# Kernel tuning notes

Hardware: AMD Instinct MI355X
Metric: run time of the kernel (lower is better)

## Reference

```python
import jax, jax.numpy as jnp
import numpy as np

B, L, T = 16, 256, 256
ENC, DEC, MEL, SPK = 256, 1024, 80, 256
ATT, FILT, K = 128, 32, 31


def setup_inputs() -> dict:
    key = jax.random.key(0)
    ks = jax.random.split(key, 32)
    s = 0.05
    r = lambda k, shape: jax.random.normal(k, shape, dtype=jnp.float32) * s
    return {
        'encoder_outputs': jax.random.normal(ks[0], (B, L, ENC), dtype=jnp.float32),
        'speaker_embed': jax.random.normal(ks[1], (B, SPK), dtype=jnp.float32),
        'mels': jax.random.normal(ks[2], (B, T, MEL), dtype=jnp.float32),
        # prenet
        'W_pre1': r(ks[3], (DEC, MEL)), 'b_pre1': jnp.zeros((DEC,), jnp.float32),
        'W_pre2': r(ks[4], (DEC, DEC)), 'b_pre2': jnp.zeros((DEC,), jnp.float32),
        # speaker projection
        'W_sp': r(ks[5], (DEC, SPK)), 'b_sp': jnp.zeros((DEC,), jnp.float32),
        # location-sensitive attention (Tacotron-2 style)
        'W_q': r(ks[6], (ATT, DEC)),
        'W_m': r(ks[7], (ATT, ENC)),
        'W_loc_conv': r(ks[8], (FILT, 2, K)),
        'W_loc': r(ks[9], (ATT, FILT)),
        'v_att': r(ks[10], (ATT,)),
        # LSTM cells
        'W_ih1': r(ks[11], (4 * DEC, DEC + ENC)), 'W_hh1': r(ks[12], (4 * DEC, DEC)),
        'b_ih1': jnp.zeros((4 * DEC,), jnp.float32), 'b_hh1': jnp.zeros((4 * DEC,), jnp.float32),
        'W_ih2': r(ks[13], (4 * DEC, DEC)), 'W_hh2': r(ks[14], (4 * DEC, DEC)),
        'b_ih2': jnp.zeros((4 * DEC,), jnp.float32), 'b_hh2': jnp.zeros((4 * DEC,), jnp.float32),
        # output projections
        'W_mel': r(ks[15], (MEL, DEC)), 'b_mel': jnp.zeros((MEL,), jnp.float32),
        'W_stop': r(ks[16], (1, DEC)), 'b_stop': jnp.zeros((1,), jnp.float32),
    }


def _lstm_cell(x, h, c, W_ih, W_hh, b_ih, b_hh):
    g = x @ W_ih.T + h @ W_hh.T + b_ih + b_hh
    i, f, gg, o = jnp.split(g, 4, axis=-1)
    c2 = jax.nn.sigmoid(f) * c + jax.nn.sigmoid(i) * jnp.tanh(gg)
    h2 = jax.nn.sigmoid(o) * jnp.tanh(c2)
    return h2, c2


def reference(encoder_outputs, speaker_embed, mels,
              W_pre1, b_pre1, W_pre2, b_pre2, W_sp, b_sp,
              W_q, W_m, W_loc_conv, W_loc, v_att,
              W_ih1, W_hh1, b_ih1, b_hh1, W_ih2, W_hh2, b_ih2, b_hh2,
              W_mel, b_mel, W_stop, b_stop):
    b = encoder_outputs.shape[0]
    proc_mem = jnp.einsum('bld,ad->bla', encoder_outputs, W_m)  # [B,L,ATT]
    spk = speaker_embed @ W_sp.T + b_sp                          # [B,DEC]
    # teacher forcing: step 0 uses zeros, step i>0 uses mels[:, i] (matches torch loop)
    prev_mel_seq = jnp.concatenate([jnp.zeros_like(mels[:, :1]), mels[:, 1:]], axis=1)
    prev_mel_seq = prev_mel_seq.transpose(1, 0, 2)               # [T,B,MEL]

    def step(carry, prev_mel):
        h1, c1, h2, c2, prev_w, cum_w = carry
        # prenet (dropout = identity in eval)
        p = jax.nn.relu(prev_mel @ W_pre1.T + b_pre1)
        p = jax.nn.relu(p @ W_pre2.T + b_pre2)
        q = p + spk
        # location features over [prev, cumulative] attention weights
        loc = jnp.stack([prev_w, cum_w], axis=1)                 # [B,2,L]
        f = jax.lax.conv_general_dilated(loc, W_loc_conv, (1,), [(K // 2, K // 2)],
                                         dimension_numbers=('NCH', 'OIH', 'NCH'))  # [B,FILT,L]
        e = jnp.einsum('bla,a->bl', jnp.tanh((q @ W_q.T)[:, None, :]
                                             + jnp.einsum('bcl,ac->bla', f, W_loc)
                                             + proc_mem), v_att)  # [B,L]
        w = jax.nn.softmax(e, axis=1)
        ctx = jnp.einsum('bl,bld->bd', w, encoder_outputs)        # [B,ENC]
        h1n, c1n = _lstm_cell(jnp.concatenate([p, ctx], axis=1), h1, c1, W_ih1, W_hh1, b_ih1, b_hh1)
        h2n, c2n = _lstm_cell(h1n, h2, c2, W_ih2, W_hh2, b_ih2, b_hh2)
        mel = h2n @ W_mel.T + b_mel
        stop = jax.nn.sigmoid(h2n @ W_stop.T + b_stop)
        return (h1n, c1n, h2n, c2n, w, cum_w + w), (mel, stop)

    z = lambda d: jnp.zeros((b, d), jnp.float32)
    carry0 = (z(DEC), z(DEC), z(DEC), z(DEC), z(L), z(L))
    _, (mel_seq, stop_seq) = jax.lax.scan(step, carry0, prev_mel_seq)
    return mel_seq.transpose(1, 0, 2), stop_seq.transpose(1, 0, 2)
```

## Files before the change

kernel.cpp:

```cpp
#include <hip/hip_runtime.h>


namespace {

constexpr int TT = 256, BB = 16, LL = 256, MELD = 80, FILTD = 32, KC = 31;
constexpr int P1 = 2304;
constexpr int P2 = 2048;
constexpr int REDOFF = 32768;

typedef float f32x4 __attribute__((ext_vector_type(4)));

struct Args {
  const float *enc, *spe, *mels;
  const float *Wpre1, *bpre1, *Wpre2, *bpre2, *Wsp, *bsp;
  const float *Wq, *Wm, *Wconv, *Wloc, *vatt;
  const float *Wih1, *Whh1, *bih1, *bhh1;
  const float *Wih2, *Whh2, *bih2, *bhh2;
  const float *Wmel, *bmel, *Wstop, *bstop;
  float *p, *X, *qp2, *pm2, *prevmel;
  float *h1a, *h1b, *c1, *h2a, *h2b, *c2;
  float *cum, *wexp, *uctx, *pctx, *psum, *spkvec, *spkq;
  float *W81, *b81, *tmp;
  int *slots, *epoch, *pslots, *pepoch;
  float *out;
};

__device__ __forceinline__ float fast_tanh(float x) {
  float ax = fabsf(x);
  float e = __expf(-2.f * ax);
  float t = (1.f - e) / (1.f + e);
  return copysignf(t, x);
}
__device__ __forceinline__ float fast_sig(float x) { return 1.f / (1.f + __expf(-x)); }

__device__ __forceinline__ int cldi(const int* p) {
  int v;
  asm volatile("global_load_dword %0, %1, off sc0 sc1\n\ts_waitcnt vmcnt(0)"
               : "=v"(v) : "v"(p) : "memory");
  return v;
}
__device__ __forceinline__ void cst1(float* p, float v) {
  asm volatile("global_store_dword %0, %1, off sc0 sc1" :: "v"(p), "v"(v) : "memory");
}
__device__ __forceinline__ void csti(int* p, int v) {
  asm volatile("global_store_dword %0, %1, off sc0 sc1" :: "v"(p), "v"(v) : "memory");
}

__device__ __forceinline__ void bar_lgkm() {
  asm volatile("s_waitcnt lgkmcnt(0)" ::: "memory");
  __builtin_amdgcn_s_barrier();
  __builtin_amdgcn_sched_barrier(0);
}

__device__ __forceinline__ void glls(const float* g, float* l) {
  __builtin_amdgcn_global_load_lds((const __attribute__((address_space(1))) void*)g,
                                   (__attribute__((address_space(3))) void*)l, 16, 0, 0);
}

__device__ __forceinline__ void gridbar(int* slots, int* epoch, int target) {
  __syncthreads();
  if (blockIdx.x == 0) {
    if (threadIdx.x == 0) csti(&slots[0], target);
    while (cldi(&slots[threadIdx.x * 32]) < target) __builtin_amdgcn_s_sleep(1);
    __syncthreads();
    if (threadIdx.x == 0) csti(epoch, target);
  } else {
    if (threadIdx.x == 0) {
      csti(&slots[blockIdx.x * 32], target);
      while (cldi(epoch) < target) __builtin_amdgcn_s_sleep(8);
    }
  }
  __builtin_amdgcn_fence(__ATOMIC_ACQUIRE, "agent");
  __syncthreads();
}

__global__ void k_init(float* base, int n) {
  int i = blockIdx.x * blockDim.x + threadIdx.x;
  if (i < n) base[i] = 0.f;
}

__global__ void k_setpsum(float* psum) {
  if (threadIdx.x < 16) psum[256 + threadIdx.x * 16] = 1.f;
}

__global__ void k_prevmel(Args a) {
  int i = blockIdx.x * blockDim.x + threadIdx.x;
  if (i >= TT * BB * MELD) return;
  int m = i % MELD;
  int tb = i / MELD;
  int b = tb & 15, t = tb >> 4;
  a.prevmel[i] = (t == 0) ? 0.f : a.mels[(b * TT + t) * MELD + m];
}

__global__ void k_spkvec(Args a) {
  int i = blockIdx.x * blockDim.x + threadIdx.x;
  if (i >= BB * 1024) return;
  int b = i >> 10, j = i & 1023;
  const float* x = a.spe + b * 256;
  const float* w = a.Wsp + j * 256;
  float s = a.bsp[j];
  for (int k = 0; k < 256; ++k) s += x[k] * w[k];
  a.spkvec[i] = s;
}

__global__ void k_spkq(Args a) {
  int i = blockIdx.x * blockDim.x + threadIdx.x;
  if (i >= BB * 128) return;
  int b = i >> 7, q = i & 127;
  const float* x = a.spkvec + b * 1024;
  const float* w = a.Wq + q * 1024;
  float s = 0.f;
  for (int k = 0; k < 1024; ++k) s += x[k] * w[k];
  a.spkq[i] = s;
}

__global__ void k_prep81(Args a) {
  int i = blockIdx.x * blockDim.x + threadIdx.x;
  if (i < 81 * 1024) {
    int r = i >> 10, k = i & 1023;
    a.W81[i] = (r < 80) ? a.Wmel[r * 1024 + k] : a.Wstop[k];
  }
  if (i < 81) a.b81[i] = (i < 80) ? a.bmel[i] : a.bstop[0];
}

__global__ __launch_bounds__(256) void k_gemm(const float* __restrict__ A,
                                              const float* __restrict__ Bm,
                                              const float* __restrict__ bias,
                                              float* __restrict__ C,
                                              int M, int N, int K, int act) {
  __shared__ __align__(16) float As[16][132];
  __shared__ __align__(16) float Bs[16][68];
  const int bm = blockIdx.y * 128, bn = blockIdx.x * 64;
  const int tid = threadIdx.x;
  const int tm = (tid >> 4) * 8, tn = (tid & 15) * 4;
  float acc[8][4] = {};
  for (int k0 = 0; k0 < K; k0 += 16) {
    for (int i = tid; i < 512; i += 256) {
      int m = i >> 2, kq = i & 3;
      float4 v = *(const float4*)(A + (size_t)(bm + m) * K + k0 + kq * 4);
      As[kq * 4 + 0][m] = v.x; As[kq * 4 + 1][m] = v.y;
      As[kq * 4 + 2][m] = v.z; As[kq * 4 + 3][m] = v.w;
    }
    {
      int m = tid >> 2, kq = tid & 3;
      float4 v = *(const float4*)(Bm + (size_t)(bn + m) * K + k0 + kq * 4);
      Bs[kq * 4 + 0][m] = v.x; Bs[kq * 4 + 1][m] = v.y;
      Bs[kq * 4 + 2][m] = v.z; Bs[kq * 4 + 3][m] = v.w;
    }
    __syncthreads();
#pragma unroll
    for (int kk = 0; kk < 16; ++kk) {
      float4 a0 = *(const float4*)&As[kk][tm];
      float4 a1 = *(const float4*)&As[kk][tm + 4];
      float4 b0 = *(const float4*)&Bs[kk][tn];
      float av[8] = {a0.x, a0.y, a0.z, a0.w, a1.x, a1.y, a1.z, a1.w};
      float bv[4] = {b0.x, b0.y, b0.z, b0.w};
#pragma unroll
      for (int i = 0; i < 8; ++i)
#pragma unroll
        for (int j = 0; j < 4; ++j) acc[i][j] += av[i] * bv[j];
    }
    __syncthreads();
  }
#pragma unroll
  for (int i = 0; i < 8; ++i)
#pragma unroll
    for (int j = 0; j < 4; ++j) {
      float v = acc[i][j];
      if (bias) v += bias[bn + tn + j];
      if (act == 1) v = fmaxf(v, 0.f);
      C[(size_t)(bm + tm + i) * N + bn + tn + j] = v;
    }
}

__global__ void k_pm_transpose(Args a) {
  int i = blockIdx.x * blockDim.x + threadIdx.x;
  if (i >= BB * 128 * LL) return;
  int l = i & 255;
  int rest = i >> 8;
  int q = rest & 127, b = rest >> 7;
  a.pm2[i] = a.X[(size_t)((b << 8) + l) * 128 + q];
}

__global__ void k_addspkq(Args a) {
  int i = blockIdx.x * blockDim.x + threadIdx.x;
  if (i >= TT * BB * 128) return;
  int q = i & 127, b = (i >> 7) & 15;
  a.qp2[i] += a.spkq[b * 128 + q];
}

__global__ __launch_bounds__(256, 1) void k_persist(Args a) {
  __shared__ __align__(16) float xs[16 * P1];
  __shared__ __align__(16) float asc[720];
  __shared__ __align__(16) float gbuf2[280];
  const int wg = blockIdx.x, tid = threadIdx.x;
  const int wv = tid >> 6, lane = tid & 63;
  const int d0 = wg * 4, kl = lane * 4;
  const int ag = tid & 15, ll = tid >> 4;

  float* loc0 = asc;
  float* loc1 = asc + 64;
  float* aF   = asc + 128;
  float* expv = asc + 704;

  float4 wL1[9][4];
  float4 wL2[8][4];
#pragma unroll
  for (int q = 0; q < 4; ++q) {
    const int row = wv * 1024 + d0 + q;
    const float* rih1 = a.Wih1 + (size_t)row * 1280;
    const float* rhh1 = a.Whh1 + (size_t)row * 1024;
    const float* rih2 = a.Wih2 + (size_t)row * 1024;
    const float* rhh2 = a.Whh2 + (size_t)row * 1024;
#pragma unroll
    for (int kb = 0; kb < 9; ++kb)
      wL1[kb][q] = (kb < 5) ? *(const float4*)(rih1 + kb * 256 + kl)
                            : *(const float4*)(rhh1 + kb * 256 + kl - 1280);
#pragma unroll
    for (int kb = 0; kb < 8; ++kb)
      wL2[kb][q] = (kb < 4) ? *(const float4*)(rih2 + kb * 256 + kl)
                            : *(const float4*)(rhh2 + kb * 256 + kl - 1024);
  }
  const int row_r = wv * 1024 + d0 + (lane >> 4);
  const float bsum1 = a.bih1[row_r] + a.bhh1[row_r];
  const float bsum2 = a.bih2[row_r] + a.bhh2[row_r];

  const int bH = wg >> 4, cH = wg & 15, l0H = cH << 4, lH = l0H + ll;
  float pmv[8], va[8];
  {
    const float* pmb = a.pm2 + (size_t)bH * 32768;
#pragma unroll
    for (int j = 0; j < 8; ++j) {
      pmv[j] = pmb[(size_t)(ag * 8 + j) * 256 + lH];
      va[j] = a.vatt[ag * 8 + j];
    }
  }
  float ev[16];
  {
    const float* eb = a.enc + (size_t)((bH << 8) + l0H) * 256 + tid;
#pragma unroll
    for (int l2 = 0; l2 < 16; ++l2) ev[l2] = eb[l2 * 256];
  }

  float c1v = 0.f, c2v = 0.f;
  __syncthreads();

  for (int t = 0; t < 259; ++t) {
    const int cur = t & 1, prv = cur ^ 1;

    if (wg < 16 && t >= 1 && t <= 256) {
      const int par = (t - 1) & 1, b = wg;
      float sm;
      {
        const f32x4* ps4 = (const f32x4*)(a.psum + par * 256 + b * 16);
        f32x4 p0 = ps4[0], p1 = ps4[1], p2 = ps4[2], p3 = ps4[3];
        sm = (p0[0] + p0[1] + p0[2] + p0[3]) + (p1[0] + p1[1] + p1[2] + p1[3]) +
             (p2[0] + p2[1] + p2[2] + p2[3]) + (p3[0] + p3[1] + p3[2] + p3[3]);
      }
      const float inv = 1.f / sm;
      const float* pc = a.pctx + par * 65536 + b * 4096 + tid;
      float acc = 0.f;
#pragma unroll
      for (int i = 0; i < 16; ++i) acc += pc[i * 256];
      cst1(a.uctx + par * 4096 + b * 256 + tid, acc * inv);
    }

    float qpm[8], wf[8];
    if (t < 256) {
      float sm;
      {
        const f32x4* ps4 = (const f32x4*)(a.psum + prv * 256 + bH * 16);
        f32x4 p0 = ps4[0], p1 = ps4[1], p2 = ps4[2], p3 = ps4[3];
        sm = (p0[0] + p0[1] + p0[2] + p0[3]) + (p1[0] + p1[1] + p1[2] + p1[3]) +
             (p2[0] + p2[1] + p2[2] + p2[3]) + (p3[0] + p3[1] + p3[2] + p3[3]);
      }
      const float inv_ps = 1.f / sm;
      {
        const float* qpb = a.qp2 + ((size_t)(t << 4) + bH) * 128 + ag * 8;
        float4 q0 = *(const float4*)qpb;
        float4 q1 = *(const float4*)(qpb + 4);
        qpm[0] = q0.x + pmv[0]; qpm[1] = q0.y + pmv[1];
        qpm[2] = q0.z + pmv[2]; qpm[3] = q0.w + pmv[3];
        qpm[4] = q1.x + pmv[4]; qpm[5] = q1.y + pmv[5];
        qpm[6] = q1.z + pmv[6]; qpm[7] = q1.w + pmv[7];
      }
      if (tid < 64) {
        int lp = l0H - 16 + tid;
        bool ok = (lp >= 0 && lp < LL);
        float we = 0.f, cm = 0.f;
        if (ok) {
          we = a.wexp[prv * 4096 + bH * 256 + lp];
          cm = a.cum[prv * 4096 + bH * 256 + lp];
        }
        float wn = we * inv_ps;
        loc0[tid] = wn;
        loc1[tid] = ok ? (cm + wn) : 0.f;
      }
      bar_lgkm();
      if (tid < 16) cst1(a.cum + cur * 4096 + bH * 256 + l0H + tid, loc1[16 + tid]);
      for (int idx = tid; idx < FILTD * 16; idx += 256) {
        int fc = idx >> 4, ll2 = idx & 15;
        const float* w = a.Wconv + fc * 62;
        float s = 0.f;
#pragma unroll
        for (int k = 0; k < KC; ++k) {
          s += w[k] * loc0[ll2 + k + 1];
          s += w[31 + k] * loc1[ll2 + k + 1];
        }
        aF[ll2 * 36 + fc] = s;
      }
      bar_lgkm();
      {
        const float* ftr = aF + ll * 36;
        f32x4 f[8];
#pragma unroll
        for (int c4 = 0; c4 < 8; ++c4) f[c4] = *(const f32x4*)(ftr + c4 * 4);
#pragma unroll
        for (int j = 0; j < 8; ++j) {
          const float* wl = a.Wloc + (ag * 8 + j) * 32;
          float x = 0.f;
#pragma unroll
          for (int c4 = 0; c4 < 8; ++c4) {
            float4 w4 = *(const float4*)(wl + c4 * 4);
            x += w4.x * f[c4][0] + w4.y * f[c4][1] + w4.z * f[c4][2] + w4.w * f[c4][3];
          }
          wf[j] = x;
        }
      }
    }

    if (t >= 2 && t <= 257) {
      const int s1 = t - 2;
      const float* pt = a.p + (size_t)s1 * 16384;
      const float* h1r = (s1 & 1) ? a.h1a : a.h1b;
      const float* uc = a.uctx + (size_t)(s1 & 1) * 4096;
#pragma unroll
      for (int k = 0; k < 16; ++k)
        glls(pt + (size_t)(tid + k * 256) * 4, xs + k * P1 + wv * 256);
#pragma unroll
      for (int k = 0; k < 4; ++k)
        glls(uc + (size_t)(tid + k * 256) * 4, xs + (k * 4 + wv) * P1 + 1024);
#pragma unroll
      for (int k = 0; k < 16; ++k)
        glls(h1r + (size_t)(tid + k * 256) * 4, xs + k * P1 + 1280 + wv * 256);
    }

    if (t < 256) {
      {
        float s = 0.f;
#pragma unroll
        for (int j = 0; j < 8; ++j) s += va[j] * fast_tanh(qpm[j] + wf[j]);
        s += __shfl_down(s, 8, 16);
        s += __shfl_down(s, 4, 16);
        s += __shfl_down(s, 2, 16);
        s += __shfl_down(s, 1, 16);
        if (ag == 0) {
          float ex = __expf(s);
          expv[ll] = ex;
          cst1(a.wexp + cur * 4096 + bH * 256 + lH, ex);
        }
      }
      bar_lgkm();
      if (tid == 0) {
        float s = 0.f;
#pragma unroll
        for (int i = 0; i < 16; ++i) s += expv[i];
        cst1(a.psum + cur * 256 + bH * 16 + cH, s);
      }
      {
        float sctx = 0.f;
#pragma unroll
        for (int l2 = 0; l2 < 16; ++l2) sctx += expv[l2] * ev[l2];
        cst1(a.pctx + cur * 65536 + (bH * 16 + cH) * 256 + tid, sctx);
      }
    }

    if (t >= 2 && t <= 257) {
      __syncthreads();
      float acc[4][16];
#pragma unroll
      for (int q = 0; q < 4; ++q)
#pragma unroll
        for (int b = 0; b < 16; ++b) acc[q][b] = 0.f;
#pragma unroll
      for (int kb = 0; kb < 9; ++kb) {
        const float* xb = xs + kb * 256 + kl;
#pragma unroll
        for (int b = 0; b < 16; ++b) {
          float4 x4 = *(const float4*)(xb + b * P1);
#pragma unroll
          for (int q = 0; q < 4; ++q) {
            acc[q][b] += wL1[kb][q].x * x4.x;
            acc[q][b] += wL1[kb][q].y * x4.y;
            acc[q][b] += wL1[kb][q].z * x4.z;
            acc[q][b] += wL1[kb][q].w * x4.w;
          }
        }
      }
#pragma unroll
      for (int q = 0; q < 4; ++q)
#pragma unroll
        for (int b = 0; b < 16; ++b) {
          float v = acc[q][b];
          v += __shfl_xor(v, 32);
          v += __shfl_xor(v, 16);
          acc[q][b] = v;
        }
      bar_lgkm();
      if (lane < 16) {
        float* rb = xs + REDOFF + wv * 1024 + lane * 64;
        const int sx = lane << 2;
#pragma unroll
        for (int q = 0; q < 4; ++q)
#pragma unroll
          for (int bg = 0; bg < 4; ++bg) {
            f32x4 v = {acc[q][bg * 4 + 0], acc[q][bg * 4 + 1],
                       acc[q][bg * 4 + 2], acc[q][bg * 4 + 3]};
            *(f32x4*)(rb + ((q * 16 + bg * 4) ^ sx)) = v;
          }
      }
    }

    if (t >= 3) {
      const int s2 = t - 3;
      const float* h1s = (s2 & 1) ? a.h1b : a.h1a;
      const float* h2r = (s2 & 1) ? a.h2a : a.h2b;
#pragma unroll
      for (int k = 0; k < 16; ++k)
        glls(h1s + (size_t)(tid + k * 256) * 4, xs + k * P2 + wv * 256);
#pragma unroll
      for (int k = 0; k < 16; ++k)
        glls(h2r + (size_t)(tid + k * 256) * 4, xs + k * P2 + 1024 + wv * 256);
    }

    if (t >= 2 && t <= 257) {
      float* h1w = ((t - 2) & 1) ? a.h1b : a.h1a;
      {
        const int lo = lane & ~3, li = lane & 3;
        const float* rbase = xs + REDOFF + wv * 1024;
        float g = bsum1;
#pragma unroll
        for (int k = 0; k < 16; ++k) g += rbase[k * 64 + (lo ^ (k << 2)) + li];
        gbuf2[wv * 68 + lane] = g;
      }
      bar_lgkm();
      if (tid < 64) {
        int dd = tid >> 4, b = tid & 15, d = d0 + dd;
        float gi = gbuf2[0 * 68 + tid], gf = gbuf2[1 * 68 + tid];
        float gg = gbuf2[2 * 68 + tid], go = gbuf2[3 * 68 + tid];
        float cn = fast_sig(gf) * c1v + fast_sig(gi) * fast_tanh(gg);
        float hn = fast_sig(go) * fast_tanh(cn);
        c1v = cn;
        cst1(h1w + b * 1024 + d, hn);
      }
    }

    if (t >= 3) {
      const int s2 = t - 3;
      float* h2w = (s2 & 1) ? a.h2b : a.h2a;
      __syncthreads();
      float acc[4][16];
#pragma unroll
      for (int q = 0; q < 4; ++q)
#pragma unroll
        for (int b = 0; b < 16; ++b) acc[q][b] = 0.f;
#pragma unroll
      for (int kb = 0; kb < 8; ++kb) {
        const float* xb = xs + kb * 256 + kl;
#pragma unroll
        for (int b = 0; b < 16; ++b) {
          float4 x4 = *(const float4*)(xb + b * P2);
#pragma unroll
          for (int q = 0; q < 4; ++q) {
            acc[q][b] += wL2[kb][q].x * x4.x;
            acc[q][b] += wL2[kb][q].y * x4.y;
            acc[q][b] += wL2[kb][q].z * x4.z;
            acc[q][b] += wL2[kb][q].w * x4.w;
          }
        }
      }
#pragma unroll
      for (int q = 0; q < 4; ++q)
#pragma unroll
        for (int b = 0; b < 16; ++b) {
          float v = acc[q][b];
          v += __shfl_xor(v, 32);
          v += __shfl_xor(v, 16);
          acc[q][b] = v;
        }
      if (lane < 16) {
        float* rb = xs + REDOFF + wv * 1024 + lane * 64;
        const int sx = lane << 2;
#pragma unroll
        for (int q = 0; q < 4; ++q)
#pragma unroll
          for (int bg = 0; bg < 4; ++bg) {
            f32x4 v = {acc[q][bg * 4 + 0], acc[q][bg * 4 + 1],
                       acc[q][bg * 4 + 2], acc[q][bg * 4 + 3]};
            *(f32x4*)(rb + ((q * 16 + bg * 4) ^ sx)) = v;
          }
      }
      {
        const int lo = lane & ~3, li = lane & 3;
        const float* rbase = xs + REDOFF + wv * 1024;
        float g = bsum2;
#pragma unroll
        for (int k = 0; k < 16; ++k) g += rbase[k * 64 + (lo ^ (k << 2)) + li];
        gbuf2[wv * 68 + lane] = g;
      }
      bar_lgkm();
      if (tid < 64) {
        int dd = tid >> 4, b = tid & 15, d = d0 + dd;
        float gi = gbuf2[0 * 68 + tid], gf = gbuf2[1 * 68 + tid];
        float gg = gbuf2[2 * 68 + tid], go = gbuf2[3 * 68 + tid];
        float cn = fast_sig(gf) * c2v + fast_sig(gi) * fast_tanh(gg);
        float hn = fast_sig(go) * fast_tanh(cn);
        c2v = cn;
        cst1(h2w + b * 1024 + d, hn);
        a.X[(size_t)(s2 * 16 + b) * 1024 + d] = hn;
      }
    }

    if (t < 258) gridbar(a.slots, a.epoch, t + 1);
  }
}

__global__ void k_finish(Args a) {
  int i = blockIdx.x * blockDim.x + threadIdx.x;
  if (i >= 4096 * 128) return;
  int col = i & 127, tb = i >> 7;
  int t = tb >> 4, b = tb & 15;
  float v = a.tmp[i];
  if (col < 80) a.out[(size_t)(b * 256 + t) * 80 + col] = v;
  else if (col == 80) a.out[327680 + b * 256 + t] = fast_sig(v);
}

}

extern "C" void kernel_launch(void* const* d_in, const int* in_sizes, int n_in,
                              void* d_out, int out_size, void* d_ws, size_t ws_size,
                              hipStream_t stream) {
  float* ws = (float*)d_ws;
  Args a;
  a.enc = (const float*)d_in[0];
  a.spe = (const float*)d_in[1];
  a.mels = (const float*)d_in[2];
  a.Wpre1 = (const float*)d_in[3];  a.bpre1 = (const float*)d_in[4];
  a.Wpre2 = (const float*)d_in[5];  a.bpre2 = (const float*)d_in[6];
  a.Wsp = (const float*)d_in[7];    a.bsp = (const float*)d_in[8];
  a.Wq = (const float*)d_in[9];     a.Wm = (const float*)d_in[10];
  a.Wconv = (const float*)d_in[11]; a.Wloc = (const float*)d_in[12];
  a.vatt = (const float*)d_in[13];
  a.Wih1 = (const float*)d_in[14];  a.Whh1 = (const float*)d_in[15];
  a.bih1 = (const float*)d_in[16];  a.bhh1 = (const float*)d_in[17];
  a.Wih2 = (const float*)d_in[18];  a.Whh2 = (const float*)d_in[19];
  a.bih2 = (const float*)d_in[20];  a.bhh2 = (const float*)d_in[21];
  a.Wmel = (const float*)d_in[22];  a.bmel = (const float*)d_in[23];
  a.Wstop = (const float*)d_in[24]; a.bstop = (const float*)d_in[25];

  a.p    = ws + 0;
  a.X    = ws + 4194304;
  a.qp2  = ws + 8388608;
  a.pm2  = ws + 8912896;
  float* st = ws + 9437184;
  a.h1a = st + 0;      a.h1b = st + 16384;
  a.c1  = st + 32768;
  a.h2a = st + 49152;  a.h2b = st + 65536;
  a.c2  = st + 81920;
  a.cum  = st + 98304;
  a.wexp = st + 106496;
  a.uctx = st + 114688;
  a.pctx = st + 122880;
  a.psum = st + 253952;
  a.slots  = (int*)(st + 254464);
  a.epoch  = (int*)(st + 262656);
  a.pslots = (int*)(st + 262688);
  a.pepoch = (int*)(st + 270880);
  a.spkvec = ws + 9708096;
  a.spkq   = ws + 9724480;
  a.W81    = ws + 9726528;
  a.b81    = ws + 9857600;
  a.tmp    = ws + 9857728;
  a.prevmel = a.tmp;
  a.out = (float*)d_out;

  k_init<<<(270912 + 255) / 256, 256, 0, stream>>>(st, 270912);
  k_setpsum<<<1, 64, 0, stream>>>(a.psum);
  k_prevmel<<<(TT * BB * MELD + 255) / 256, 256, 0, stream>>>(a);
  k_spkvec<<<(BB * 1024 + 255) / 256, 256, 0, stream>>>(a);
  k_spkq<<<(BB * 128 + 255) / 256, 256, 0, stream>>>(a);
  k_prep81<<<(81 * 1024 + 255) / 256, 256, 0, stream>>>(a);

  k_gemm<<<dim3(16, 32), 256, 0, stream>>>(a.prevmel, a.Wpre1, a.bpre1, a.X, 4096, 1024, 80, 1);
  k_gemm<<<dim3(16, 32), 256, 0, stream>>>(a.X, a.Wpre2, a.bpre2, a.p, 4096, 1024, 1024, 1);
  k_gemm<<<dim3(2, 32), 256, 0, stream>>>(a.p, a.Wq, nullptr, a.qp2, 4096, 128, 1024, 0);
  k_addspkq<<<(TT * BB * 128 + 255) / 256, 256, 0, stream>>>(a);
  k_gemm<<<dim3(2, 32), 256, 0, stream>>>(a.enc, a.Wm, nullptr, a.X, 4096, 128, 256, 0);
  k_pm_transpose<<<(BB * 128 * LL + 255) / 256, 256, 0, stream>>>(a);

  {
    void* kargs[] = {(void*)&a};
    hipError_t e = hipLaunchCooperativeKernel(reinterpret_cast<const void*>(&k_persist),
                                              dim3(256), dim3(256), kargs, 0, stream);
    if (e != hipSuccess) k_persist<<<256, 256, 0, stream>>>(a);
  }

  k_gemm<<<dim3(2, 32), 256, 0, stream>>>(a.X, a.W81, a.b81, a.tmp, 4096, 128, 1024, 0);
  k_finish<<<(4096 * 128 + 255) / 256, 256, 0, stream>>>(a);
}
```

Before: 15.37 ms.

## Use 32-deep ring buffers for recurrent state to skip most grid-barrier acquire fences

Replaces the double-buffered h1/h2/uctx/psum state with 32-slot ring buffers indexed by timestep. The per-step agent-scope acquire fence (cache invalidate) in the grid barrier now runs only every 16 steps. Cross-block reads of pctx, wexp and cum switch to coherent sc0/sc1 loads so they stay fresh without the fence. The aim is to cut cache-invalidation cost on every step of the persistent kernel. The risk is correctness: any remaining cached (non-coherent) read of data written by another block, such as the plain psum loads, could return stale values between fences.

```diff
diff --git a/kernel.cpp b/kernel.cpp
--- a/kernel.cpp
+++ b/kernel.cpp
@@ -18,10 +18,10 @@
   const float *Wih2, *Whh2, *bih2, *bhh2;
   const float *Wmel, *bmel, *Wstop, *bstop;
   float *p, *X, *qp2, *pm2, *prevmel;
-  float *h1a, *h1b, *c1, *h2a, *h2b, *c2;
-  float *cum, *wexp, *uctx, *pctx, *psum, *spkvec, *spkq;
+  float *cum, *wexp, *pctx, *spkvec, *spkq;
+  float *h1d, *h2d, *uctxd, *psumd;
   float *W81, *b81, *tmp;
-  int *slots, *epoch, *pslots, *pepoch;
+  int *slots, *epoch;
   float *out;
 };
 
@@ -45,6 +45,34 @@
 __device__ __forceinline__ void csti(int* p, int v) {
   asm volatile("global_store_dword %0, %1, off sc0 sc1" :: "v"(p), "v"(v) : "memory");
 }
+__device__ __forceinline__ void cld2(float* d0, float* d1, const float* q0,
+                                     const float* q1) {
+  float x, y;
+  asm volatile(
+      "global_load_dword %0, %2, off sc0 sc1\n\t"
+      "global_load_dword %1, %3, off sc0 sc1\n\t"
+      "s_waitcnt vmcnt(0)"
+      : "=&v"(x), "=&v"(y) : "v"(q0), "v"(q1) : "memory");
+  *d0 = x; *d1 = y;
+}
+__device__ __forceinline__ void cld8d(float d[8], const float* q0, const float* q1,
+                                      const float* q2, const float* q3, const float* q4,
+                                      const float* q5, const float* q6, const float* q7) {
+  asm volatile(
+      "global_load_dword %0, %8, off sc0 sc1\n\t"
+      "global_load_dword %1, %9, off sc0 sc1\n\t"
+      "global_load_dword %2, %10, off sc0 sc1\n\t"
+      "global_load_dword %3, %11, off sc0 sc1\n\t"
+      "global_load_dword %4, %12, off sc0 sc1\n\t"
+      "global_load_dword %5, %13, off sc0 sc1\n\t"
+      "global_load_dword %6, %14, off sc0 sc1\n\t"
+      "global_load_dword %7, %15, off sc0 sc1\n\t"
+      "s_waitcnt vmcnt(0)"
+      : "=&v"(d[0]), "=&v"(d[1]), "=&v"(d[2]), "=&v"(d[3]),
+        "=&v"(d[4]), "=&v"(d[5]), "=&v"(d[6]), "=&v"(d[7])
+      : "v"(q0), "v"(q1), "v"(q2), "v"(q3), "v"(q4), "v"(q5), "v"(q6), "v"(q7)
+      : "memory");
+}
 
 __device__ __forceinline__ void bar_lgkm() {
   asm volatile("s_waitcnt lgkmcnt(0)" ::: "memory");
@@ -57,7 +85,7 @@
                                    (__attribute__((address_space(3))) void*)l, 16, 0, 0);
 }
 
-__device__ __forceinline__ void gridbar(int* slots, int* epoch, int target) {
+__device__ __forceinline__ void gridbar(int* slots, int* epoch, int target, bool inv) {
   __syncthreads();
   if (blockIdx.x == 0) {
     if (threadIdx.x == 0) csti(&slots[0], target);
@@ -70,7 +98,7 @@
       while (cldi(epoch) < target) __builtin_amdgcn_s_sleep(8);
     }
   }
-  __builtin_amdgcn_fence(__ATOMIC_ACQUIRE, "agent");
+  if (inv) __builtin_amdgcn_fence(__ATOMIC_ACQUIRE, "agent");
   __syncthreads();
 }
 
@@ -79,8 +107,8 @@
   if (i < n) base[i] = 0.f;
 }
 
-__global__ void k_setpsum(float* psum) {
-  if (threadIdx.x < 16) psum[256 + threadIdx.x * 16] = 1.f;
+__global__ void k_setpsum(float* psumd) {
+  if (threadIdx.x < 16) psumd[threadIdx.x * 16] = 1.f;
 }
 
 __global__ void k_prevmel(Args a) {
@@ -252,24 +280,31 @@
       const int par = (t - 1) & 1, b = wg;
       float sm;
       {
-        const f32x4* ps4 = (const f32x4*)(a.psum + par * 256 + b * 16);
+        const f32x4* ps4 = (const f32x4*)(a.psumd + (size_t)(t & 31) * 256 + b * 16);
         f32x4 p0 = ps4[0], p1 = ps4[1], p2 = ps4[2], p3 = ps4[3];
         sm = (p0[0] + p0[1] + p0[2] + p0[3]) + (p1[0] + p1[1] + p1[2] + p1[3]) +
              (p2[0] + p2[1] + p2[2] + p2[3]) + (p3[0] + p3[1] + p3[2] + p3[3]);
       }
       const float inv = 1.f / sm;
       const float* pc = a.pctx + par * 65536 + b * 4096 + tid;
+      float d[8];
       float acc = 0.f;
-#pragma unroll
-      for (int i = 0; i < 16; ++i) acc += pc[i * 256];
-      cst1(a.uctx + par * 4096 + b * 256 + tid, acc * inv);
+      cld8d(d, pc, pc + 256, pc + 512, pc + 768, pc + 1024, pc + 1280, pc + 1536,
+            pc + 1792);
+#pragma unroll
+      for (int i = 0; i < 8; ++i) acc += d[i];
+      cld8d(d, pc + 2048, pc + 2304, pc + 2560, pc + 2816, pc + 3072, pc + 3328,
+            pc + 3584, pc + 3840);
+#pragma unroll
+      for (int i = 0; i < 8; ++i) acc += d[i];
+      cst1(a.uctxd + (size_t)(t & 31) * 4096 + b * 256 + tid, acc * inv);
     }
 
     float qpm[8], wf[8];
     if (t < 256) {
       float sm;
       {
-        const f32x4* ps4 = (const f32x4*)(a.psum + prv * 256 + bH * 16);
+        const f32x4* ps4 = (const f32x4*)(a.psumd + (size_t)(t & 31) * 256 + bH * 16);
         f32x4 p0 = ps4[0], p1 = ps4[1], p2 = ps4[2], p3 = ps4[3];
         sm = (p0[0] + p0[1] + p0[2] + p0[3]) + (p1[0] + p1[1] + p1[2] + p1[3]) +
              (p2[0] + p2[1] + p2[2] + p2[3]) + (p3[0] + p3[1] + p3[2] + p3[3]);
@@ -288,10 +323,9 @@
         int lp = l0H - 16 + tid;
         bool ok = (lp >= 0 && lp < LL);
         float we = 0.f, cm = 0.f;
-        if (ok) {
-          we = a.wexp[prv * 4096 + bH * 256 + lp];
-          cm = a.cum[prv * 4096 + bH * 256 + lp];
-        }
+        if (ok)
+          cld2(&we, &cm, a.wexp + prv * 4096 + bH * 256 + lp,
+               a.cum + prv * 4096 + bH * 256 + lp);
         float wn = we * inv_ps;
         loc0[tid] = wn;
         loc1[tid] = ok ? (cm + wn) : 0.f;
@@ -332,8 +366,8 @@
     if (t >= 2 && t <= 257) {
       const int s1 = t - 2;
       const float* pt = a.p + (size_t)s1 * 16384;
-      const float* h1r = (s1 & 1) ? a.h1a : a.h1b;
-      const float* uc = a.uctx + (size_t)(s1 & 1) * 4096;
+      const float* h1r = a.h1d + (size_t)(s1 & 31) * 16384;
+      const float* uc = a.uctxd + (size_t)((s1 + 1) & 31) * 4096;
 #pragma unroll
       for (int k = 0; k < 16; ++k)
         glls(pt + (size_t)(tid + k * 256) * 4, xs + k * P1 + wv * 256);
@@ -365,7 +399,7 @@
         float s = 0.f;
 #pragma unroll
         for (int i = 0; i < 16; ++i) s += expv[i];
-        cst1(a.psum + cur * 256 + bH * 16 + cH, s);
+        cst1(a.psumd + (size_t)((t + 1) & 31) * 256 + bH * 16 + cH, s);
       }
       {
         float sctx = 0.f;
@@ -423,8 +457,8 @@
 
     if (t >= 3) {
       const int s2 = t - 3;
-      const float* h1s = (s2 & 1) ? a.h1b : a.h1a;
-      const float* h2r = (s2 & 1) ? a.h2a : a.h2b;
+      const float* h1s = a.h1d + (size_t)((s2 + 1) & 31) * 16384;
+      const float* h2r = a.h2d + (size_t)(s2 & 31) * 16384;
 #pragma unroll
       for (int k = 0; k < 16; ++k)
         glls(h1s + (size_t)(tid + k * 256) * 4, xs + k * P2 + wv * 256);
@@ -434,7 +468,8 @@
     }
 
     if (t >= 2 && t <= 257) {
-      float* h1w = ((t - 2) & 1) ? a.h1b : a.h1a;
+      const int s1 = t - 2;
+      float* h1w = a.h1d + (size_t)((s1 + 1) & 31) * 16384;
       {
         const int lo = lane & ~3, li = lane & 3;
         const float* rbase = xs + REDOFF + wv * 1024;
@@ -457,7 +492,7 @@
 
     if (t >= 3) {
       const int s2 = t - 3;
-      float* h2w = (s2 & 1) ? a.h2b : a.h2a;
+      float* h2w = a.h2d + (size_t)((s2 + 1) & 31) * 16384;
       __syncthreads();
       float acc[4][16];
 #pragma unroll
@@ -521,7 +556,7 @@
       }
     }
 
-    if (t < 258) gridbar(a.slots, a.epoch, t + 1);
+    if (t < 258) gridbar(a.slots, a.epoch, t + 1, (t & 15) == 15);
   }
 }
 
@@ -563,29 +598,28 @@
   a.qp2  = ws + 8388608;
   a.pm2  = ws + 8912896;
   float* st = ws + 9437184;
-  a.h1a = st + 0;      a.h1b = st + 16384;
-  a.c1  = st + 32768;
-  a.h2a = st + 49152;  a.h2b = st + 65536;
-  a.c2  = st + 81920;
   a.cum  = st + 98304;
   a.wexp = st + 106496;
-  a.uctx = st + 114688;
   a.pctx = st + 122880;
-  a.psum = st + 253952;
   a.slots  = (int*)(st + 254464);
   a.epoch  = (int*)(st + 262656);
-  a.pslots = (int*)(st + 262688);
-  a.pepoch = (int*)(st + 270880);
   a.spkvec = ws + 9708096;
   a.spkq   = ws + 9724480;
   a.W81    = ws + 9726528;
   a.b81    = ws + 9857600;
   a.tmp    = ws + 9857728;
   a.prevmel = a.tmp;
+  a.h1d   = ws + 10382016;
+  a.h2d   = ws + 10906304;
+  a.uctxd = ws + 11430592;
+  a.psumd = ws + 11561664;
   a.out = (float*)d_out;
 
   k_init<<<(270912 + 255) / 256, 256, 0, stream>>>(st, 270912);
-  k_setpsum<<<1, 64, 0, stream>>>(a.psum);
+  k_init<<<64, 256, 0, stream>>>(a.h1d, 16384);
+  k_init<<<64, 256, 0, stream>>>(a.h2d, 16384);
+  k_init<<<1, 256, 0, stream>>>(a.psumd, 256);
+  k_setpsum<<<1, 64, 0, stream>>>(a.psumd);
   k_prevmel<<<(TT * BB * MELD + 255) / 256, 256, 0, stream>>>(a);
   k_spkvec<<<(BB * 1024 + 255) / 256, 256, 0, stream>>>(a);
   k_spkq<<<(BB * 128 + 255) / 256, 256, 0, stream>>>(a);
```

After: 14.12 ms. -8.1%, faster.
